# Kernel tuning notes

Measured on AMD Instinct MI355X. Metric: run time of the kernel, lower is better.

## Reference

```python
import jax, jax.numpy as jnp
import numpy as np

N_NODES = 100000
N_EDGES = 1600000
D_FEAT = 128
HIDDEN = 256


def setup_inputs() -> dict:
    key = jax.random.key(0)
    k1, k2, k3, k4, k5, k6, k7 = jax.random.split(key, 7)
    h = jax.random.normal(k1, (N_NODES, D_FEAT), dtype=jnp.float32)
    src = jax.random.randint(k2, (N_EDGES,), 0, N_NODES, dtype=jnp.int64)
    dst = jax.random.randint(k3, (N_EDGES,), 0, N_NODES, dtype=jnp.int64)
    # Linear weights, torch layout: W [out, in], b [out]
    lim1 = 1.0 / np.sqrt(2 * D_FEAT)
    W1_w = jax.random.uniform(k4, (HIDDEN, 2 * D_FEAT), minval=-lim1, maxval=lim1, dtype=jnp.float32)
    W1_b = jax.random.uniform(k5, (HIDDEN,), minval=-lim1, maxval=lim1, dtype=jnp.float32)
    lim2 = 1.0 / np.sqrt(HIDDEN)
    W2_w = jax.random.uniform(k6, (1, HIDDEN), minval=-lim2, maxval=lim2, dtype=jnp.float32)
    W2_b = jax.random.uniform(k7, (1,), minval=-lim2, maxval=lim2, dtype=jnp.float32)
    return {"h": h, "src": src, "dst": dst, "W1_w": W1_w, "W1_b": W1_b, "W2_w": W2_w, "W2_b": W2_b}


def reference(h, src, dst, W1_w, W1_b, W2_w, W2_b):
    # gather per-edge src/dst node features and concat: [E, 2D]
    x = jnp.concatenate([h[src], h[dst]], axis=1)
    # Linear -> ReLU -> Linear, squeeze last dim -> [E]
    hid = jax.nn.relu(x @ W1_w.T + W1_b)          # [E, H]
    score = (hid @ W2_w.T + W2_b)[:, 0]           # [E]
    return score
```

## Files before the change

### kernel.cpp

```cpp
#include <hip/hip_runtime.h>


#define NNODES 100000
#define E_TOTAL 1600000
#define D 128
#define K2 256
#define H 256

typedef short bf16x8 __attribute__((ext_vector_type(8)));
typedef short bf16x4 __attribute__((ext_vector_type(4)));
typedef float f32x4 __attribute__((ext_vector_type(4)));
typedef const __attribute__((address_space(1))) unsigned short* gas_t;
typedef __attribute__((address_space(3))) unsigned short* las_t;

__device__ __forceinline__ unsigned short f2bf(float f) {
    unsigned u = __float_as_uint(f);
    u += 0x7fff + ((u >> 16) & 1);
    return (unsigned short)(u >> 16);
}
__device__ __forceinline__ float bf2f(unsigned short s) {
    return __uint_as_float((unsigned)s << 16);
}


__global__ __launch_bounds__(256, 2) void u_gemm(
    const float* __restrict__ h,
    const float* __restrict__ W1,
    const float* __restrict__ b1,
    unsigned short* __restrict__ Us,
    unsigned short* __restrict__ Ud)
{
    __shared__ __align__(16) unsigned short A[64 * 136];
    __shared__ __align__(16) unsigned short S[64 * 268];

    const int tid = threadIdx.x;
    const int wave = tid >> 6;
    const int lane = tid & 63;
    const int l15 = lane & 15;
    const int quad = lane >> 4;

    const int r0 = blockIdx.x * 64;
    int rows = NNODES - r0; if (rows > 64) rows = 64;

    const float4* hf4 = (const float4*)(h + (size_t)r0 * D);
    const int lim = rows * 32;
#pragma unroll
    for (int i = 0; i < 8; ++i) {
        int j = tid + i * 256;
        if (j < lim) {
            float4 v = hf4[j];
            bf16x4 b;
            b[0] = (short)f2bf(v.x); b[1] = (short)f2bf(v.y);
            b[2] = (short)f2bf(v.z); b[3] = (short)f2bf(v.w);
            *(bf16x4*)&A[(j >> 5) * 136 + (j & 31) * 4] = b;
        }
    }
    __syncthreads();

    for (int half = 0; half < 2; ++half) {
        const int koff = half * 128;
        unsigned short* U = half ? Ud : Us;

        bf16x8 B[4][4];
        float bias[4];
#pragma unroll
        for (int nt = 0; nt < 4; ++nt) {
            const int n = wave * 64 + nt * 16 + l15;
            bias[nt] = half ? 0.f : b1[n];
#pragma unroll
            for (int kit = 0; kit < 4; ++kit) {
                const float* wp = W1 + (size_t)n * K2 + koff + kit * 32 + quad * 8;
                float4 x = *(const float4*)wp;
                float4 y = *(const float4*)(wp + 4);
                bf16x8 f;
                f[0] = (short)f2bf(x.x); f[1] = (short)f2bf(x.y);
                f[2] = (short)f2bf(x.z); f[3] = (short)f2bf(x.w);
                f[4] = (short)f2bf(y.x); f[5] = (short)f2bf(y.y);
                f[6] = (short)f2bf(y.z); f[7] = (short)f2bf(y.w);
                B[kit][nt] = f;
            }
        }

        f32x4 acc[4][4];
        const f32x4 zero = {0.f, 0.f, 0.f, 0.f};
#pragma unroll
        for (int ms = 0; ms < 4; ++ms)
#pragma unroll
            for (int nt = 0; nt < 4; ++nt)
                acc[ms][nt] = zero;

#pragma unroll
        for (int kit = 0; kit < 4; ++kit) {
            bf16x8 a[4];
#pragma unroll
            for (int ms = 0; ms < 4; ++ms)
                a[ms] = *(const bf16x8*)&A[(ms * 16 + l15) * 136 + kit * 32 + quad * 8];
#pragma unroll
            for (int ms = 0; ms < 4; ++ms)
#pragma unroll
                for (int nt = 0; nt < 4; ++nt)
                    acc[ms][nt] = __builtin_amdgcn_mfma_f32_16x16x32_bf16(
                        a[ms], B[kit][nt], acc[ms][nt], 0, 0, 0);
        }

        if (half) __syncthreads();
#pragma unroll
        for (int ms = 0; ms < 4; ++ms)
#pragma unroll
            for (int r = 0; r < 4; ++r) {
                const int m = ms * 16 + quad * 4 + r;
#pragma unroll
                for (int nt = 0; nt < 4; ++nt)
                    S[m * 268 + wave * 64 + nt * 16 + l15] =
                        f2bf(acc[ms][nt][r] + bias[nt]);
            }
        __syncthreads();

#pragma unroll
        for (int i = 0; i < 8; ++i) {
            const int j = i * 256 + tid;
            const int row = j >> 5;
            const int cc = j & 31;
            if (row < rows) {
                bf16x8 vv = *(const bf16x8*)&S[row * 268 + cc * 8];
                *(bf16x8*)(U + (size_t)(r0 + row) * H + cc * 8) = vv;
            }
        }
    }
}

__global__ __launch_bounds__(256) void edge_score(
    const unsigned short* __restrict__ Us,
    const unsigned short* __restrict__ Ud,
    const int* __restrict__ srcE,
    const int* __restrict__ dstE,
    const float* __restrict__ w2,
    const float* __restrict__ b2p,
    float* __restrict__ out)
{
    const int gt = blockIdx.x * 256 + threadIdx.x;
    const int l = gt & 15;
    const int q = gt >> 4;
    const int Q = (gridDim.x * 256) >> 4;
    const int NGRP = E_TOTAL / 4;

    float w2v[16];
#pragma unroll
    for (int j = 0; j < 16; ++j) w2v[j] = w2[l * 16 + j];
    const float b2 = *b2p;

    for (int g = q; g < NGRP; g += Q) {
        const int e0 = g * 4;
        const int4 s4 = *(const int4*)(srcE + e0);
        const int4 d4 = *(const int4*)(dstE + e0);
        const int sv[4] = {s4.x, s4.y, s4.z, s4.w};
        const int dv[4] = {d4.x, d4.y, d4.z, d4.w};

        bf16x8 u[4][2], v[4][2];
#pragma unroll
        for (int k = 0; k < 4; ++k) {
            const bf16x8* us = (const bf16x8*)(Us + (size_t)sv[k] * H + l * 16);
            const bf16x8* ud = (const bf16x8*)(Ud + (size_t)dv[k] * H + l * 16);
            u[k][0] = us[0]; u[k][1] = us[1];
            v[k][0] = ud[0]; v[k][1] = ud[1];
        }

        float4 res;
        float* resp = (float*)&res;
#pragma unroll
        for (int k = 0; k < 4; ++k) {
            float acc = 0.f;
#pragma unroll
            for (int j = 0; j < 8; ++j) {
                float hv = bf2f((unsigned short)u[k][0][j]) + bf2f((unsigned short)v[k][0][j]);
                acc = fmaf(fmaxf(hv, 0.f), w2v[j], acc);
            }
#pragma unroll
            for (int j = 0; j < 8; ++j) {
                float hv = bf2f((unsigned short)u[k][1][j]) + bf2f((unsigned short)v[k][1][j]);
                acc = fmaf(fmaxf(hv, 0.f), w2v[j + 8], acc);
            }
            acc += __shfl_xor(acc, 1, 16);
            acc += __shfl_xor(acc, 2, 16);
            acc += __shfl_xor(acc, 4, 16);
            acc += __shfl_xor(acc, 8, 16);
            resp[k] = acc + b2;
        }
        if (l == 0) *(float4*)(out + e0) = res;
    }
}


#define TILE_M 32
#define NTILES (E_TOTAL / TILE_M)
#define GRID 2500

#if defined(__has_attribute)
#if __has_attribute(amdgpu_waves_per_eu)
#define LB __launch_bounds__(256) __attribute__((amdgpu_waves_per_eu(2, 2)))
#else
#define LB __launch_bounds__(256, 2)
#endif
#else
#define LB __launch_bounds__(256, 2)
#endif

__global__ void cvt_kernel(const float* __restrict__ h, const float* __restrict__ w1,
                           unsigned short* __restrict__ hbf, unsigned short* __restrict__ w1bf,
                           int n4h, int n4w) {
    int i = blockIdx.x * blockDim.x + threadIdx.x;
    const float* s; unsigned short* d; int j;
    if (i < n4h) { s = h; d = hbf; j = i; }
    else if (i < n4h + n4w) { s = w1; d = w1bf; j = i - n4h; }
    else return;
    float4 v = ((const float4*)s)[j];
    ushort4 o;
    o.x = f2bf(v.x); o.y = f2bf(v.y); o.z = f2bf(v.z); o.w = f2bf(v.w);
    ((ushort4*)d)[j] = o;
}

__global__ LB void edge_mlp(
    const unsigned short* __restrict__ hbf,
    const int* __restrict__ srcE,
    const int* __restrict__ dstE,
    const unsigned short* __restrict__ w1bf,
    const float* __restrict__ b1,
    const float* __restrict__ w2,
    const float* __restrict__ b2p,
    float* __restrict__ out)
{
    __shared__ __align__(16) unsigned short X[2][TILE_M * K2];
    __shared__ float red[2][TILE_M][5];

    const int tid = threadIdx.x;
    const int wave = tid >> 6;
    const int lane = tid & 63;
    const int lane15 = lane & 15;
    const int quad = lane >> 4;

    bf16x8 B[8][4];
#pragma unroll
    for (int kit = 0; kit < 8; ++kit)
#pragma unroll
        for (int nt = 0; nt < 4; ++nt) {
            int n = wave * 64 + nt * 16 + lane15;
            int k = kit * 32 + quad * 8;
            B[kit][nt] = *(const bf16x8*)(w1bf + n * K2 + k);
        }

    float b1v[4], w2v[4];
#pragma unroll
    for (int nt = 0; nt < 4; ++nt) {
        int n = wave * 64 + nt * 16 + lane15;
        b1v[nt] = b1[n];
        w2v[nt] = w2[n];
    }
    const float b2 = *b2p;

    const int r_off = tid >> 5;
    const int c = (tid & 31) ^ (r_off & 7);
    const int half = c >> 4;
    const int fc = c & 15;
    const int* idx_base = half ? dstE : srcE;
    const int gshort = fc * 8;

    const int t0 = blockIdx.x;
    int inode[4];

#pragma unroll
    for (int it = 0; it < 4; ++it)
        inode[it] = idx_base[t0 * TILE_M + it * 8 + r_off];
#pragma unroll
    for (int it = 0; it < 4; ++it)
        __builtin_amdgcn_global_load_lds(
            (gas_t)(hbf + inode[it] * D + gshort),
            (las_t)(&X[0][0] + it * 2048 + wave * 512), 16, 0, 0);
    {
        const int t1 = t0 + GRID;
#pragma unroll
        for (int it = 0; it < 4; ++it)
            inode[it] = idx_base[t1 * TILE_M + it * 8 + r_off];
    }

    int buf = 0;
    int prev_eb = -1;

    for (int tile = t0; tile < NTILES; tile += GRID) {
        __syncthreads();

        const int nt1 = tile + GRID;
        if (nt1 < NTILES) {
            unsigned short* Xn = &X[buf ^ 1][0];
#pragma unroll
            for (int it = 0; it < 4; ++it)
                __builtin_amdgcn_global_load_lds(
                    (gas_t)(hbf + inode[it] * D + gshort),
                    (las_t)(Xn + it * 2048 + wave * 512), 16, 0, 0);
        }
        const int nt2 = tile + 2 * GRID;
        if (nt2 < NTILES) {
            const int eb2 = nt2 * TILE_M;
#pragma unroll
            for (int it = 0; it < 4; ++it)
                inode[it] = idx_base[eb2 + it * 8 + r_off];
        }
        if (prev_eb >= 0 && tid < TILE_M) {
            float s = b2;
#pragma unroll
            for (int w = 0; w < 4; ++w) s += red[buf ^ 1][tid][w];
            out[prev_eb + tid] = s;
        }

        const unsigned short* Xc = &X[buf][0];
        f32x4 acc[2][4];
        const f32x4 zero = {0.f, 0.f, 0.f, 0.f};
#pragma unroll
        for (int ms = 0; ms < 2; ++ms)
#pragma unroll
            for (int nt = 0; nt < 4; ++nt)
                acc[ms][nt] = zero;

#pragma unroll
        for (int kit = 0; kit < 8; ++kit) {
            const int p8 = (((kit * 4 + quad) ^ (lane15 & 7))) * 8;
            bf16x8 a[2];
#pragma unroll
            for (int ms = 0; ms < 2; ++ms)
                a[ms] = *(const bf16x8*)&Xc[(ms * 16 + lane15) * K2 + p8];
#pragma unroll
            for (int ms = 0; ms < 2; ++ms)
#pragma unroll
                for (int nt = 0; nt < 4; ++nt)
                    acc[ms][nt] = __builtin_amdgcn_mfma_f32_16x16x32_bf16(
                        a[ms], B[kit][nt], acc[ms][nt], 0, 0, 0);
        }

#pragma unroll
        for (int ms = 0; ms < 2; ++ms)
#pragma unroll
            for (int r = 0; r < 4; ++r) {
                float p = 0.f;
#pragma unroll
                for (int nt = 0; nt < 4; ++nt) {
                    float hv = acc[ms][nt][r] + b1v[nt];
                    p = fmaf(fmaxf(hv, 0.f), w2v[nt], p);
                }
                p += __shfl_xor(p, 1, 16);
                p += __shfl_xor(p, 2, 16);
                p += __shfl_xor(p, 4, 16);
                p += __shfl_xor(p, 8, 16);
                if (lane15 == 0) red[buf][ms * 16 + quad * 4 + r][wave] = p;
            }
        prev_eb = tile * TILE_M;
        buf ^= 1;
    }

    __syncthreads();
    if (prev_eb >= 0 && tid < TILE_M) {
        float s = b2;
#pragma unroll
        for (int w = 0; w < 4; ++w) s += red[buf ^ 1][tid][w];
        out[prev_eb + tid] = s;
    }
}


extern "C" void kernel_launch(void* const* d_in, const int* in_sizes, int n_in,
                              void* d_out, int out_size, void* d_ws, size_t ws_size,
                              hipStream_t stream) {
    const float* h    = (const float*)d_in[0];
    const int*   srcE = (const int*)d_in[1];
    const int*   dstE = (const int*)d_in[2];
    const float* W1   = (const float*)d_in[3];
    const float* b1   = (const float*)d_in[4];
    const float* w2   = (const float*)d_in[5];
    const float* b2   = (const float*)d_in[6];
    float* out = (float*)d_out;

    const size_t planeElems = (size_t)NNODES * H;
    const size_t need = planeElems * 2 * sizeof(unsigned short);

    if (ws_size >= need) {
        unsigned short* Us = (unsigned short*)d_ws;
        unsigned short* Ud = Us + planeElems;
        u_gemm<<<(NNODES + 63) / 64, 256, 0, stream>>>(h, W1, b1, Us, Ud);
        edge_score<<<4096, 256, 0, stream>>>(Us, Ud, srcE, dstE, w2, b2, out);
    } else {
        unsigned short* hbf  = (unsigned short*)d_ws;
        unsigned short* w1bf = hbf + (size_t)NNODES * D;
        int n4h = NNODES * D / 4;
        int n4w = H * K2 / 4;
        int n4 = n4h + n4w;
        cvt_kernel<<<(n4 + 255) / 256, 256, 0, stream>>>(h, W1, hbf, w1bf, n4h, n4w);
        edge_mlp<<<GRID, 256, 0, stream>>>(hbf, srcE, dstE, w1bf, b1, w2, b2, out);
    }
}
```

Baseline: 385.1 us.

## Sort edges by source node via counting sort to reuse source rows

Adds a histogram, a single-block scan and an atomic scatter that bucket the edges by source node into CSR order. The edge kernel then assigns 16 lanes per source node, loads that node's precomputed Us row once and gathers only the Ud rows for its edges. W1 is also converted to bf16 once in a small kernel instead of inside every u_gemm block. The aim is to halve the random gather traffic, at the cost of several extra launches, a serial 1024-thread scan over 100k nodes, atomic contention, scattered output writes and load imbalance across nodes with different degrees.

```diff
diff --git a/kernel.cpp b/kernel.cpp
--- a/kernel.cpp
+++ b/kernel.cpp
@@ -22,10 +22,18 @@
     return __uint_as_float((unsigned)s << 16);
 }
 
+__global__ void cvt_w1(const float* __restrict__ W1, unsigned short* __restrict__ w1bf, int n4) {
+    int i = blockIdx.x * blockDim.x + threadIdx.x;
+    if (i >= n4) return;
+    float4 v = ((const float4*)W1)[i];
+    ushort4 o;
+    o.x = f2bf(v.x); o.y = f2bf(v.y); o.z = f2bf(v.z); o.w = f2bf(v.w);
+    ((ushort4*)w1bf)[i] = o;
+}
 
 __global__ __launch_bounds__(256, 2) void u_gemm(
     const float* __restrict__ h,
-    const float* __restrict__ W1,
+    const unsigned short* __restrict__ w1bf,
     const float* __restrict__ b1,
     unsigned short* __restrict__ Us,
     unsigned short* __restrict__ Ud)
@@ -68,17 +76,8 @@
             const int n = wave * 64 + nt * 16 + l15;
             bias[nt] = half ? 0.f : b1[n];
 #pragma unroll
-            for (int kit = 0; kit < 4; ++kit) {
-                const float* wp = W1 + (size_t)n * K2 + koff + kit * 32 + quad * 8;
-                float4 x = *(const float4*)wp;
-                float4 y = *(const float4*)(wp + 4);
-                bf16x8 f;
-                f[0] = (short)f2bf(x.x); f[1] = (short)f2bf(x.y);
-                f[2] = (short)f2bf(x.z); f[3] = (short)f2bf(x.w);
-                f[4] = (short)f2bf(y.x); f[5] = (short)f2bf(y.y);
-                f[6] = (short)f2bf(y.z); f[7] = (short)f2bf(y.w);
-                B[kit][nt] = f;
-            }
+            for (int kit = 0; kit < 4; ++kit)
+                B[kit][nt] = *(const bf16x8*)(w1bf + (size_t)n * K2 + koff + kit * 32 + quad * 8);
         }
 
         f32x4 acc[4][4];
@@ -129,64 +128,111 @@
     }
 }
 
-__global__ __launch_bounds__(256) void edge_score(
+__global__ void hist_kernel(const int* __restrict__ srcE, int* __restrict__ bins) {
+    int i = blockIdx.x * blockDim.x + threadIdx.x;
+    if (i < E_TOTAL) atomicAdd(&bins[srcE[i]], 1);
+}
+
+__global__ void scan_kernel(int* __restrict__ cursor, int* __restrict__ starts) {
+    __shared__ int s[1024];
+    __shared__ int sbase;
+    const int tid = threadIdx.x;
+    if (tid == 0) sbase = 0;
+    __syncthreads();
+    const int NCH = (NNODES + 1023) / 1024;
+    for (int c = 0; c < NCH; ++c) {
+        const int i = c * 1024 + tid;
+        const int x = (i < NNODES) ? cursor[i] : 0;
+        s[tid] = x;
+        __syncthreads();
+        for (int off = 1; off < 1024; off <<= 1) {
+            int t = (tid >= off) ? s[tid - off] : 0;
+            __syncthreads();
+            s[tid] += t;
+            __syncthreads();
+        }
+        const int incl = s[tid];
+        const int total = s[1023];
+        const int b = sbase;
+        if (i < NNODES) {
+            starts[i] = b + incl - x;
+            cursor[i] = b + incl - x;
+        }
+        __syncthreads();
+        if (tid == 0) sbase = b + total;
+        __syncthreads();
+    }
+    if (tid == 0) starts[NNODES] = sbase;
+}
+
+__global__ void scatter_kernel(const int* __restrict__ srcE, const int* __restrict__ dstE,
+                               int* __restrict__ cursor, int2* __restrict__ sorted) {
+    int i = blockIdx.x * blockDim.x + threadIdx.x;
+    if (i >= E_TOTAL) return;
+    int pos = atomicAdd(&cursor[srcE[i]], 1);
+    int2 p; p.x = dstE[i]; p.y = i;
+    sorted[pos] = p;
+}
+
+__global__ __launch_bounds__(256) void edge_score_sorted(
     const unsigned short* __restrict__ Us,
     const unsigned short* __restrict__ Ud,
-    const int* __restrict__ srcE,
-    const int* __restrict__ dstE,
+    const int* __restrict__ starts,
+    const int2* __restrict__ sorted,
     const float* __restrict__ w2,
     const float* __restrict__ b2p,
     float* __restrict__ out)
 {
     const int gt = blockIdx.x * 256 + threadIdx.x;
     const int l = gt & 15;
-    const int q = gt >> 4;
-    const int Q = (gridDim.x * 256) >> 4;
-    const int NGRP = E_TOTAL / 4;
+    const int v = gt >> 4;
+    if (v >= NNODES) return;
 
     float w2v[16];
 #pragma unroll
     for (int j = 0; j < 16; ++j) w2v[j] = w2[l * 16 + j];
     const float b2 = *b2p;
 
-    for (int g = q; g < NGRP; g += Q) {
-        const int e0 = g * 4;
-        const int4 s4 = *(const int4*)(srcE + e0);
-        const int4 d4 = *(const int4*)(dstE + e0);
-        const int sv[4] = {s4.x, s4.y, s4.z, s4.w};
-        const int dv[4] = {d4.x, d4.y, d4.z, d4.w};
-
-        bf16x8 u[4][2], v[4][2];
+    const int s0 = starts[v];
+    const int s1 = starts[v + 1];
+    if (s0 >= s1) return;
+
+    const bf16x8* us = (const bf16x8*)(Us + (size_t)v * H + l * 16);
+    const bf16x8 u0 = us[0], u1 = us[1];
+
+    for (int base = s0; base < s1; base += 4) {
+        int K = s1 - base; if (K > 4) K = 4;
+        int2 p[4];
+        bf16x8 vv[4][2];
+#pragma unroll
+        for (int k = 0; k < 4; ++k)
+            if (k < K) p[k] = sorted[base + k];
+#pragma unroll
+        for (int k = 0; k < 4; ++k)
+            if (k < K) {
+                const bf16x8* ud = (const bf16x8*)(Ud + (size_t)p[k].x * H + l * 16);
+                vv[k][0] = ud[0]; vv[k][1] = ud[1];
+            }
 #pragma unroll
         for (int k = 0; k < 4; ++k) {
-            const bf16x8* us = (const bf16x8*)(Us + (size_t)sv[k] * H + l * 16);
-            const bf16x8* ud = (const bf16x8*)(Ud + (size_t)dv[k] * H + l * 16);
-            u[k][0] = us[0]; u[k][1] = us[1];
-            v[k][0] = ud[0]; v[k][1] = ud[1];
-        }
-
-        float4 res;
-        float* resp = (float*)&res;
-#pragma unroll
-        for (int k = 0; k < 4; ++k) {
+            if (k >= K) break;
             float acc = 0.f;
 #pragma unroll
             for (int j = 0; j < 8; ++j) {
-                float hv = bf2f((unsigned short)u[k][0][j]) + bf2f((unsigned short)v[k][0][j]);
+                float hv = bf2f((unsigned short)u0[j]) + bf2f((unsigned short)vv[k][0][j]);
                 acc = fmaf(fmaxf(hv, 0.f), w2v[j], acc);
             }
 #pragma unroll
             for (int j = 0; j < 8; ++j) {
-                float hv = bf2f((unsigned short)u[k][1][j]) + bf2f((unsigned short)v[k][1][j]);
+                float hv = bf2f((unsigned short)u1[j]) + bf2f((unsigned short)vv[k][1][j]);
                 acc = fmaf(fmaxf(hv, 0.f), w2v[j + 8], acc);
             }
             acc += __shfl_xor(acc, 1, 16);
             acc += __shfl_xor(acc, 2, 16);
             acc += __shfl_xor(acc, 4, 16);
             acc += __shfl_xor(acc, 8, 16);
-            resp[k] = acc + b2;
-        }
-        if (l == 0) *(float4*)(out + e0) = res;
+            if (l == 0) out[p[k].y] = acc + b2;
+        }
     }
 }
 
@@ -377,14 +423,33 @@
     const float* b2   = (const float*)d_in[6];
     float* out = (float*)d_out;
 
-    const size_t planeElems = (size_t)NNODES * H;
-    const size_t need = planeElems * 2 * sizeof(unsigned short);
+    char* ws = (char*)d_ws;
+    const size_t offUs     = 0;
+    const size_t offUd     = 51200000;
+    const size_t offSorted = 102400000;
+    const size_t offW1bf   = 115200000;
+    const size_t offStarts = 115331072;
+    const size_t offCursor = 115731080;
+    const size_t need      = offCursor + 400000;
 
     if (ws_size >= need) {
-        unsigned short* Us = (unsigned short*)d_ws;
-        unsigned short* Ud = Us + planeElems;
-        u_gemm<<<(NNODES + 63) / 64, 256, 0, stream>>>(h, W1, b1, Us, Ud);
-        edge_score<<<4096, 256, 0, stream>>>(Us, Ud, srcE, dstE, w2, b2, out);
+        unsigned short* Us    = (unsigned short*)(ws + offUs);
+        unsigned short* Ud    = (unsigned short*)(ws + offUd);
+        int2*           sorted= (int2*)(ws + offSorted);
+        unsigned short* w1bf  = (unsigned short*)(ws + offW1bf);
+        int*            starts= (int*)(ws + offStarts);
+        int*            cursor= (int*)(ws + offCursor);
+
+        cvt_w1<<<(H * K2 / 4 + 255) / 256, 256, 0, stream>>>(W1, w1bf, H * K2 / 4);
+        u_gemm<<<(NNODES + 63) / 64, 256, 0, stream>>>(h, w1bf, b1, Us, Ud);
+
+        hipMemsetAsync(cursor, 0, NNODES * sizeof(int), stream);
+        hist_kernel<<<(E_TOTAL + 255) / 256, 256, 0, stream>>>(srcE, cursor);
+        scan_kernel<<<1, 1024, 0, stream>>>(cursor, starts);
+        scatter_kernel<<<(E_TOTAL + 255) / 256, 256, 0, stream>>>(srcE, dstE, cursor, sorted);
+
+        edge_score_sorted<<<(NNODES * 16 + 255) / 256, 256, 0, stream>>>(
+            Us, Ud, starts, sorted, w2, b2, out);
     } else {
         unsigned short* hbf  = (unsigned short*)d_ws;
         unsigned short* w1bf = hbf + (size_t)NNODES * D;
```

Measured after the change: 668.2 us. 1.74x slower.
